# Kernel optimization log

Hardware: AMD Instinct MI355X
Metric: run time of the kernel (lower is better)

Reference implementation:

```python
import jax, jax.numpy as jnp
import numpy as np

N_FFT = 400          # Whisper n_fft
HOP = 160            # Whisper hop_length
CUT = N_FFT // 2 + 1 # freq_cutoff = 201
T_SIG = 9_600_000    # 10 minutes @ 16 kHz


def _make_basis():
    # fourier_basis[k, n] = exp(-2*pi*i*k*n/N); keep first CUT rows,
    # stack [real; imag], multiply by periodic Hann window.
    n = jnp.arange(N_FFT, dtype=jnp.float32)
    k = jnp.arange(CUT, dtype=jnp.float32)
    ang = (2.0 * jnp.pi / N_FFT) * k[:, None] * n[None, :]          # [CUT, N_FFT]
    window = 0.5 * (1.0 - jnp.cos(2.0 * jnp.pi * n / N_FFT))        # periodic Hann
    basis = jnp.concatenate([jnp.cos(ang), -jnp.sin(ang)], axis=0)  # [2*CUT, N_FFT]
    return (basis * window[None, :]).astype(jnp.float32)


def setup_inputs() -> dict:
    key = jax.random.key(0)
    signal = jax.random.normal(key, (T_SIG,), dtype=jnp.float32)
    basis = _make_basis()  # conv weight, exact DFT basis (frozen in original)
    return {"signal": signal, "basis": basis}


def reference(signal, basis):
    # zero-pad by freq_cutoff-1 on each side, then strided conv == windowed DFT
    pad = CUT - 1
    x = jnp.pad(signal, (pad, pad))[None, None, :]          # [1, 1, T+2*pad]
    w = basis[:, None, :]                                    # [2*CUT, 1, N_FFT]
    y = jax.lax.conv_general_dilated(
        x, w, window_strides=(HOP,), padding='VALID',
        dimension_numbers=('NCH', 'OIH', 'NCH'))             # [1, 2*CUT, frames]
    real = y[:, :CUT, :]
    imag = y[:, CUT:2 * CUT, :]
    return real, imag
```

## Files before the change

kernel.cpp:

```cpp
#include <hip/hip_runtime.h>

#define HOP 160
#define NROWS 402
#define NTAPS 400
#define T_SIG 9600000
#define N_FRAMES 60001
#define PAD 200

#define MT 13
#define KS 26
#define FPB 128
#define MSPLIT 3
#define NBT ((N_FRAMES + FPB - 1) / FPB)
#define SPAN (127*HOP + 416)
#define SPAN4 (SPAN/4)
#define LDSE 21776

typedef __bf16 bf16x8 __attribute__((ext_vector_type(8)));
typedef float f32x16 __attribute__((ext_vector_type(16)));
typedef unsigned short u16x8 __attribute__((ext_vector_type(8)));
typedef unsigned short u16x4 __attribute__((ext_vector_type(4)));

__device__ __forceinline__ unsigned short f2bf(float f) {
    unsigned int u = __builtin_bit_cast(unsigned int, f);
    u += 0x7fffu + ((u >> 16) & 1u);
    return (unsigned short)(u >> 16);
}

__global__ void stft_prep(const float* __restrict__ basis,
                          unsigned short* __restrict__ packed) {
    int tid = blockIdx.x * 256 + threadIdx.x;
    if (tid >= MT * KS * 64) return;
    int lane = tid & 63;
    int frag = tid >> 6;
    int ks = frag % KS;
    int mt = frag / KS;
    int row = mt * 32 + (lane & 31);
    int colb = ks * 16 + (lane >> 5) * 8;
    u16x8 v;
#pragma unroll
    for (int i = 0; i < 8; ++i) {
        int col = colb + i;
        float f = (row < NROWS && col < NTAPS) ? basis[row * NTAPS + col] : 0.0f;
        v[i] = f2bf(f);
    }
    *reinterpret_cast<u16x8*>(packed + (size_t)tid * 8) = v;
}

__launch_bounds__(256, 3)
__global__ void stft_mfma(const float* __restrict__ sig,
                          const unsigned short* __restrict__ packedA,
                          float* __restrict__ out) {
    __shared__ unsigned short sl[LDSE];
    const int tid = threadIdx.x;
    const int bt = blockIdx.x % NBT;
    const int bm = blockIdx.x / NBT;
    const long sbase = (long)bt * (FPB * HOP) - PAD;

    for (int idx = tid; idx < SPAN4; idx += 256) {
        const int e = idx * 4;
        const long g0 = sbase + e;
        float4 v;
        if (g0 >= 0 && g0 + 4 <= (long)T_SIG) {
            v = *reinterpret_cast<const float4*>(sig + g0);
        } else {
            v.x = (g0 + 0 >= 0 && g0 + 0 < (long)T_SIG) ? sig[g0 + 0] : 0.0f;
            v.y = (g0 + 1 >= 0 && g0 + 1 < (long)T_SIG) ? sig[g0 + 1] : 0.0f;
            v.z = (g0 + 2 >= 0 && g0 + 2 < (long)T_SIG) ? sig[g0 + 2] : 0.0f;
            v.w = (g0 + 3 >= 0 && g0 + 3 < (long)T_SIG) ? sig[g0 + 3] : 0.0f;
        }
        u16x4 s;
        s[0] = f2bf(v.x); s[1] = f2bf(v.y); s[2] = f2bf(v.z); s[3] = f2bf(v.w);
        const int pos = e + 8 * (e / 160);
        *reinterpret_cast<u16x4*>(&sl[pos]) = s;
    }
    __syncthreads();

    const int lane = tid & 63;
    const int w = tid >> 6;
    const int l31 = lane & 31;
    const int g = lane >> 5;
    const int lf = w * 32 + l31;
    const long t = (long)bt * FPB + lf;

    const int mt0 = (bm == 0) ? 0 : 5 + 4 * (bm - 1);
    const int mtN = (bm == 0) ? 5 : 4;

    const unsigned short* bbase = &sl[lf * 168 + g * 8];
    const int rowg = 4 * g;

#pragma unroll 1
    for (int mi = 0; mi < mtN; ++mi) {
        const int mt = mt0 + mi;
        f32x16 acc = {0,0,0,0,0,0,0,0,0,0,0,0,0,0,0,0};
        const unsigned short* pA = packedA + ((size_t)(mt * KS) * 64 + lane) * 8;
#pragma unroll
        for (int ks = 0; ks < KS; ++ks) {
            const bf16x8 a = *reinterpret_cast<const bf16x8*>(pA + (size_t)ks * 64 * 8);
            const bf16x8 b = *reinterpret_cast<const bf16x8*>(bbase + ks * 16 + 8 * (ks / 10));
            acc = __builtin_amdgcn_mfma_f32_32x32x16_bf16(a, b, acc, 0, 0, 0);
        }
        if (t < N_FRAMES) {
            const int rb = mt * 32 + rowg;
#pragma unroll
            for (int r = 0; r < 16; ++r) {
                const int row = rb + (r & 3) + 8 * (r >> 2);
                if (row < NROWS) out[(long)row * N_FRAMES + t] = acc[r];
            }
        }
        __syncthreads();
    }
}

__global__ void stft_naive(const float* __restrict__ sig,
                           const float* __restrict__ basis,
                           float* __restrict__ out) {
    long idx = (long)blockIdx.x * 256 + threadIdx.x;
    if (idx >= (long)NROWS * N_FRAMES) return;
    int row = (int)(idx / N_FRAMES);
    int tt = (int)(idx % N_FRAMES);
    long s0 = (long)tt * HOP - PAD;
    float acc = 0.0f;
    for (int n = 0; n < NTAPS; ++n) {
        long s = s0 + n;
        float x = (s >= 0 && s < (long)T_SIG) ? sig[s] : 0.0f;
        acc = fmaf(x, basis[row * NTAPS + n], acc);
    }
    out[idx] = acc;
}

extern "C" void kernel_launch(void* const* d_in, const int* in_sizes, int n_in,
                              void* d_out, int out_size, void* d_ws, size_t ws_size,
                              hipStream_t stream) {
    (void)in_sizes; (void)n_in; (void)out_size;
    const float* sig = (const float*)d_in[0];
    const float* basis = (const float*)d_in[1];
    float* out = (float*)d_out;
    const size_t need = (size_t)MT * KS * 64 * 8 * sizeof(unsigned short);
    if (ws_size >= need) {
        unsigned short* packed = (unsigned short*)d_ws;
        stft_prep<<<(MT * KS * 64 + 255) / 256, 256, 0, stream>>>(basis, packed);
        stft_mfma<<<NBT * MSPLIT, 256, 0, stream>>>(sig, packed, out);
    } else {
        long total = (long)NROWS * N_FRAMES;
        stft_naive<<<(int)((total + 255) / 256), 256, 0, stream>>>(sig, basis, out);
    }
}
```

Before: 65.40 us.

## Keep basis fragments in registers per wave and loop over frame tiles

Each wave now owns one 32-row basis tile, loads all 26 A fragments into registers once, and loops over the four 32-frame tiles of the block. Previously every wave reloaded A fragments from global memory for each M tile, and the block had a per-iteration barrier. The launch changes from 3 to 4 M-groups per time block, interleaved so adjacent blocks share the same signal span. In exchange, the 26 bf16x8 fragments add heavy register pressure that may lower occupancy, and the last group has three idle waves because only 13 M tiles exist. Signal staging into LDS is now repeated four times per span instead of three.

```diff
diff --git a/kernel.cpp b/kernel.cpp
--- a/kernel.cpp
+++ b/kernel.cpp
@@ -10,7 +10,7 @@
 #define MT 13
 #define KS 26
 #define FPB 128
-#define MSPLIT 3
+#define MGROUPS 4
 #define NBT ((N_FRAMES + FPB - 1) / FPB)
 #define SPAN (127*HOP + 416)
 #define SPAN4 (SPAN/4)
@@ -53,10 +53,21 @@
                           float* __restrict__ out) {
     __shared__ unsigned short sl[LDSE];
     const int tid = threadIdx.x;
-    const int bt = blockIdx.x % NBT;
-    const int bm = blockIdx.x / NBT;
+    const int bg = blockIdx.x & (MGROUPS - 1);
+    const int bt = blockIdx.x >> 2;
+    const int lane = tid & 63;
+    const int w = tid >> 6;
+    const int mt = bg * 4 + w;
+
+    bf16x8 afr[KS];
+    if (mt < MT) {
+        const unsigned short* pA = packedA + ((size_t)(mt * KS) * 64 + lane) * 8;
+#pragma unroll
+        for (int ks = 0; ks < KS; ++ks)
+            afr[ks] = *reinterpret_cast<const bf16x8*>(pA + (size_t)ks * 512);
+    }
+
     const long sbase = (long)bt * (FPB * HOP) - PAD;
-
     for (int idx = tid; idx < SPAN4; idx += 256) {
         const int e = idx * 4;
         const long g0 = sbase + e;
@@ -76,39 +87,30 @@
     }
     __syncthreads();
 
-    const int lane = tid & 63;
-    const int w = tid >> 6;
+    if (mt >= MT) return;
+
     const int l31 = lane & 31;
     const int g = lane >> 5;
-    const int lf = w * 32 + l31;
-    const long t = (long)bt * FPB + lf;
-
-    const int mt0 = (bm == 0) ? 0 : 5 + 4 * (bm - 1);
-    const int mtN = (bm == 0) ? 5 : 4;
-
-    const unsigned short* bbase = &sl[lf * 168 + g * 8];
-    const int rowg = 4 * g;
+    const int rb = mt * 32 + 4 * g;
 
 #pragma unroll 1
-    for (int mi = 0; mi < mtN; ++mi) {
-        const int mt = mt0 + mi;
+    for (int i = 0; i < FPB / 32; ++i) {
+        const int lf = i * 32 + l31;
+        const long t = (long)bt * FPB + lf;
+        const unsigned short* bb = &sl[lf * 168 + g * 8];
         f32x16 acc = {0,0,0,0,0,0,0,0,0,0,0,0,0,0,0,0};
-        const unsigned short* pA = packedA + ((size_t)(mt * KS) * 64 + lane) * 8;
 #pragma unroll
         for (int ks = 0; ks < KS; ++ks) {
-            const bf16x8 a = *reinterpret_cast<const bf16x8*>(pA + (size_t)ks * 64 * 8);
-            const bf16x8 b = *reinterpret_cast<const bf16x8*>(bbase + ks * 16 + 8 * (ks / 10));
-            acc = __builtin_amdgcn_mfma_f32_32x32x16_bf16(a, b, acc, 0, 0, 0);
+            const bf16x8 b = *reinterpret_cast<const bf16x8*>(bb + ks * 16 + 8 * (ks / 10));
+            acc = __builtin_amdgcn_mfma_f32_32x32x16_bf16(afr[ks], b, acc, 0, 0, 0);
         }
         if (t < N_FRAMES) {
-            const int rb = mt * 32 + rowg;
 #pragma unroll
             for (int r = 0; r < 16; ++r) {
                 const int row = rb + (r & 3) + 8 * (r >> 2);
                 if (row < NROWS) out[(long)row * N_FRAMES + t] = acc[r];
             }
         }
-        __syncthreads();
     }
 }
 
@@ -140,7 +142,7 @@
     if (ws_size >= need) {
         unsigned short* packed = (unsigned short*)d_ws;
         stft_prep<<<(MT * KS * 64 + 255) / 256, 256, 0, stream>>>(basis, packed);
-        stft_mfma<<<NBT * MSPLIT, 256, 0, stream>>>(sig, packed, out);
+        stft_mfma<<<NBT * MGROUPS, 256, 0, stream>>>(sig, packed, out);
     } else {
         long total = (long)NROWS * N_FRAMES;
         stft_naive<<<(int)((total + 255) / 256), 256, 0, stream>>>(sig, basis, out);
```

After: 69.24 us. +5.9%, slower.

## Add 128x128 tiled MFMA GEMM with pre-packed bf16 signal and staged A in LDS

Applied to the files above, without the earlier changes.

Adds a new path that first converts the whole signal to padded bf16 in workspace. The basis is packed into per-block-row phases, and then a GEMM kernel computes 128 rows x 128 frames per block, with each wave holding a 2x2 grid of 32x32 MFMA accumulators. The signal tile is loaded with global_load_lds directly into LDS, and the A tiles are staged through registers into LDS in four k-phases. Compared with the old one-tile-per-wave loop, this raises operand reuse and cuts global A traffic. In exchange it needs about 20 MB of workspace and two extra prep passes over the signal, and it falls back to the old kernels when the workspace is too small.

```diff
diff --git a/kernel.cpp b/kernel.cpp
--- a/kernel.cpp
+++ b/kernel.cpp
@@ -6,6 +6,174 @@
 #define T_SIG 9600000
 #define N_FRAMES 60001
 #define PAD 200
+
+typedef __bf16 bf16x8 __attribute__((ext_vector_type(8)));
+typedef float f32x16 __attribute__((ext_vector_type(16)));
+typedef unsigned short u16x8 __attribute__((ext_vector_type(8)));
+typedef unsigned short u16x4 __attribute__((ext_vector_type(4)));
+typedef unsigned int u32x4 __attribute__((ext_vector_type(4)));
+
+__device__ __forceinline__ unsigned short f2bf(float f) {
+    unsigned int u = __builtin_bit_cast(unsigned int, f);
+    u += 0x7fffu + ((u >> 16) & 1u);
+    return (unsigned short)(u >> 16);
+}
+
+__device__ __forceinline__ void gll16(const void* g, void* l) {
+    __builtin_amdgcn_global_load_lds(
+        (const __attribute__((address_space(1))) unsigned int*)g,
+        (__attribute__((address_space(3))) unsigned int*)l, 16, 0, 0);
+}
+
+
+#define SIG_OFF 425984
+#define APH0 0
+#define APH1 28672
+#define APH2 57344
+#define APH3 81920
+#define ABM_STRIDE 106496
+#define A_LDS_B 30720
+#define SIG_LDS_B 45056
+#define NEED1 (425984UL + 20172800UL)
+
+__global__ void prep_sig(const float* __restrict__ sig,
+                         unsigned short* __restrict__ sp) {
+    long chunk = (long)blockIdx.x * 256 + threadIdx.x;
+    if (chunk >= 2401440L) return;
+    long i = chunk * 4;
+    long pos = i + 8 * (i / 160);
+    u16x4 v;
+    if (i >= 200 && i + 4 <= 9600200L) {
+        float4 f = *reinterpret_cast<const float4*>(sig + (i - 200));
+        v[0] = f2bf(f.x); v[1] = f2bf(f.y); v[2] = f2bf(f.z); v[3] = f2bf(f.w);
+    } else {
+        v[0] = v[1] = v[2] = v[3] = 0;
+    }
+    *reinterpret_cast<u16x4*>(sp + pos) = v;
+}
+
+__global__ void prep_a(const float* __restrict__ basis,
+                       unsigned short* __restrict__ ap) {
+    int s = blockIdx.x * 256 + threadIdx.x;
+    int bm = s / 6656, rem = s % 6656;
+    int sip, kb;
+    if (rem < 1792)      { sip = rem;        kb = 0;  }
+    else if (rem < 3584) { sip = rem - 1792; kb = 7;  }
+    else if (rem < 5120) { sip = rem - 3584; kb = 14; }
+    else                 { sip = rem - 5120; kb = 20; }
+    int ksg = sip >> 7, r = sip & 127;
+    int ka = kb + (ksg >> 1);
+    int k0 = ka * 16 + (ksg & 1) * 8;
+    int m = bm * 128 + r;
+    u16x8 v;
+#pragma unroll
+    for (int j = 0; j < 8; ++j) {
+        int k = k0 + j;
+        float f = (m < NROWS && k < NTAPS) ? basis[m * NTAPS + k] : 0.0f;
+        v[j] = f2bf(f);
+    }
+    *reinterpret_cast<u16x8*>(ap + (size_t)s * 8) = v;
+}
+
+#define A_LOAD(POFF, N) do { _Pragma("unroll") \
+    for (int it = 0; it < (N); ++it) { \
+        int slot = it * 256 + tid; \
+        areg[it] = *reinterpret_cast<const u32x4*>(aBase + (POFF) + slot * 16); \
+    } } while (0)
+
+#define A_WRITE(N) do { _Pragma("unroll") \
+    for (int it = 0; it < (N); ++it) { \
+        int slot = it * 256 + tid; \
+        *reinterpret_cast<u32x4*>(aB + (slot & 127) * 240 + (slot >> 7) * 16) = areg[it]; \
+    } } while (0)
+
+#define COMPUTE_PHASE(KSB, KSN) do { _Pragma("unroll") \
+    for (int i = 0; i < (KSN); ++i) { \
+        const int ka = (KSB) + i; \
+        const int sc = ka * 32 + (ka >= 10 ? 16 : 0) + (ka >= 20 ? 16 : 0); \
+        bf16x8 a0 = *reinterpret_cast<const bf16x8*>(aR0g + i * 32); \
+        bf16x8 a1 = *reinterpret_cast<const bf16x8*>(aR0g + 7680 + i * 32); \
+        bf16x8 b0 = *reinterpret_cast<const bf16x8*>(sB0 + sc); \
+        bf16x8 b1 = *reinterpret_cast<const bf16x8*>(sB0 + 10752 + sc); \
+        acc00 = __builtin_amdgcn_mfma_f32_32x32x16_bf16(a0, b0, acc00, 0, 0, 0); \
+        acc01 = __builtin_amdgcn_mfma_f32_32x32x16_bf16(a0, b1, acc01, 0, 0, 0); \
+        acc10 = __builtin_amdgcn_mfma_f32_32x32x16_bf16(a1, b0, acc10, 0, 0, 0); \
+        acc11 = __builtin_amdgcn_mfma_f32_32x32x16_bf16(a1, b1, acc11, 0, 0, 0); \
+    } } while (0)
+
+#define STORE_ACC(A, R0, T) do { if ((T) < (long)N_FRAMES) { _Pragma("unroll") \
+    for (int r = 0; r < 16; ++r) { \
+        int row = (R0) + (r & 3) + 8 * (r >> 2); \
+        if (row < NROWS) out[(long)row * N_FRAMES + (T)] = (A)[r]; \
+    } } } while (0)
+
+__launch_bounds__(256)
+__global__ void stft_gemm(const unsigned short* __restrict__ sigp,
+                          const unsigned short* __restrict__ apack,
+                          float* __restrict__ out) {
+    __shared__ __align__(16) char lds[A_LDS_B + SIG_LDS_B];
+    char* aB = lds;
+    char* sB = lds + A_LDS_B;
+    const int tid = threadIdx.x;
+    const int bm = blockIdx.x & 3;
+    const int bt = blockIdx.x >> 2;
+    const char* aBase = (const char*)apack + (size_t)bm * ABM_STRIDE;
+
+    u32x4 areg[7];
+    A_LOAD(APH0, 7);
+    {
+        const char* sg = (const char*)sigp + (size_t)bt * 43008;
+#pragma unroll
+        for (int it = 0; it < 11; ++it) {
+            int slot = it * 256 + tid;
+            gll16(sg + slot * 16, sB + slot * 16);
+        }
+    }
+    A_WRITE(7);
+    __syncthreads();
+
+    const int lane = tid & 63;
+    const int w = tid >> 6;
+    const int wm = w >> 1;
+    const int wf = w & 1;
+    const int l31 = lane & 31;
+    const int g = lane >> 5;
+
+    const char* aR0g = aB + (wm * 64 + l31) * 240 + g * 16;
+    const char* sB0 = sB + (wf * 64 + l31) * 336 + g * 16;
+
+    f32x16 acc00 = {0,0,0,0,0,0,0,0,0,0,0,0,0,0,0,0};
+    f32x16 acc01 = {0,0,0,0,0,0,0,0,0,0,0,0,0,0,0,0};
+    f32x16 acc10 = {0,0,0,0,0,0,0,0,0,0,0,0,0,0,0,0};
+    f32x16 acc11 = {0,0,0,0,0,0,0,0,0,0,0,0,0,0,0,0};
+
+    A_LOAD(APH1, 7);
+    COMPUTE_PHASE(0, 7);
+    __syncthreads();
+    A_WRITE(7);
+    __syncthreads();
+
+    A_LOAD(APH2, 6);
+    COMPUTE_PHASE(7, 7);
+    __syncthreads();
+    A_WRITE(6);
+    __syncthreads();
+
+    A_LOAD(APH3, 6);
+    COMPUTE_PHASE(14, 6);
+    __syncthreads();
+    A_WRITE(6);
+    __syncthreads();
+
+    COMPUTE_PHASE(20, 6);
+
+    const int rBase = bm * 128 + wm * 64 + 4 * g;
+    const long tBase = (long)bt * 128 + wf * 64 + l31;
+    STORE_ACC(acc00, rBase, tBase);
+    STORE_ACC(acc01, rBase, tBase + 32);
+    STORE_ACC(acc10, rBase + 32, tBase);
+    STORE_ACC(acc11, rBase + 32, tBase + 32);
+}
 
 #define MT 13
 #define KS 26
@@ -16,19 +184,8 @@
 #define SPAN4 (SPAN/4)
 #define LDSE 21776
 
-typedef __bf16 bf16x8 __attribute__((ext_vector_type(8)));
-typedef float f32x16 __attribute__((ext_vector_type(16)));
-typedef unsigned short u16x8 __attribute__((ext_vector_type(8)));
-typedef unsigned short u16x4 __attribute__((ext_vector_type(4)));
-
-__device__ __forceinline__ unsigned short f2bf(float f) {
-    unsigned int u = __builtin_bit_cast(unsigned int, f);
-    u += 0x7fffu + ((u >> 16) & 1u);
-    return (unsigned short)(u >> 16);
-}
-
-__global__ void stft_prep(const float* __restrict__ basis,
-                          unsigned short* __restrict__ packed) {
+__global__ void stft_prep2(const float* __restrict__ basis,
+                           unsigned short* __restrict__ packed) {
     int tid = blockIdx.x * 256 + threadIdx.x;
     if (tid >= MT * KS * 64) return;
     int lane = tid & 63;
@@ -48,15 +205,14 @@
 }
 
 __launch_bounds__(256, 3)
-__global__ void stft_mfma(const float* __restrict__ sig,
-                          const unsigned short* __restrict__ packedA,
-                          float* __restrict__ out) {
+__global__ void stft_mfma2(const float* __restrict__ sig,
+                           const unsigned short* __restrict__ packedA,
+                           float* __restrict__ out) {
     __shared__ unsigned short sl[LDSE];
     const int tid = threadIdx.x;
     const int bt = blockIdx.x % NBT;
-    const int bm = blockIdx.x / NBT;
+    const int bmm = blockIdx.x / NBT;
     const long sbase = (long)bt * (FPB * HOP) - PAD;
-
     for (int idx = tid; idx < SPAN4; idx += 256) {
         const int e = idx * 4;
         const long g0 = sbase + e;
@@ -75,20 +231,16 @@
         *reinterpret_cast<u16x4*>(&sl[pos]) = s;
     }
     __syncthreads();
-
     const int lane = tid & 63;
     const int w = tid >> 6;
     const int l31 = lane & 31;
     const int g = lane >> 5;
     const int lf = w * 32 + l31;
     const long t = (long)bt * FPB + lf;
-
-    const int mt0 = (bm == 0) ? 0 : 5 + 4 * (bm - 1);
-    const int mtN = (bm == 0) ? 5 : 4;
-
+    const int mt0 = (bmm == 0) ? 0 : 5 + 4 * (bmm - 1);
+    const int mtN = (bmm == 0) ? 5 : 4;
     const unsigned short* bbase = &sl[lf * 168 + g * 8];
     const int rowg = 4 * g;
-
 #pragma unroll 1
     for (int mi = 0; mi < mtN; ++mi) {
         const int mt = mt0 + mi;
@@ -96,7 +248,7 @@
         const unsigned short* pA = packedA + ((size_t)(mt * KS) * 64 + lane) * 8;
 #pragma unroll
         for (int ks = 0; ks < KS; ++ks) {
-            const bf16x8 a = *reinterpret_cast<const bf16x8*>(pA + (size_t)ks * 64 * 8);
+            const bf16x8 a = *reinterpret_cast<const bf16x8*>(pA + (size_t)ks * 512);
             const bf16x8 b = *reinterpret_cast<const bf16x8*>(bbase + ks * 16 + 8 * (ks / 10));
             acc = __builtin_amdgcn_mfma_f32_32x32x16_bf16(a, b, acc, 0, 0, 0);
         }
@@ -136,11 +288,16 @@
     const float* sig = (const float*)d_in[0];
     const float* basis = (const float*)d_in[1];
     float* out = (float*)d_out;
-    const size_t need = (size_t)MT * KS * 64 * 8 * sizeof(unsigned short);
-    if (ws_size >= need) {
+    if (ws_size >= NEED1) {
+        unsigned short* ap = (unsigned short*)d_ws;
+        unsigned short* sp = (unsigned short*)((char*)d_ws + SIG_OFF);
+        prep_sig<<<9381, 256, 0, stream>>>(sig, sp);
+        prep_a<<<104, 256, 0, stream>>>(basis, ap);
+        stft_gemm<<<469 * 4, 256, 0, stream>>>(sp, ap, out);
+    } else if (ws_size >= (size_t)MT * KS * 64 * 8 * sizeof(unsigned short)) {
         unsigned short* packed = (unsigned short*)d_ws;
-        stft_prep<<<(MT * KS * 64 + 255) / 256, 256, 0, stream>>>(basis, packed);
-        stft_mfma<<<NBT * MSPLIT, 256, 0, stream>>>(sig, packed, out);
+        stft_prep2<<<(MT * KS * 64 + 255) / 256, 256, 0, stream>>>(basis, packed);
+        stft_mfma2<<<NBT * MSPLIT, 256, 0, stream>>>(sig, packed, out);
     } else {
         long total = (long)NROWS * N_FRAMES;
         stft_naive<<<(int)((total + 255) / 256), 256, 0, stream>>>(sig, basis, out);
```

Measured after the change: 67.78 us. 3.6% more time.
